# Optimization experiments

Hardware: AMD Instinct MI355X
Metric: run time of the kernel (lower is better)

The kernel has to match this reference:

```python
import jax, jax.numpy as jnp
import numpy as np

B, L, S, D, H, E, UV = 4, 2048, 2048, 1024, 8, 128, 128
ROT_DIM = H * E  # RotaryEmbedding(dim=qk_size*n_heads) applied on flattened dim


def gelu(x):
    return jax.nn.gelu(x, approximate=False)  # torch nn.GELU default (erf)


def rope(x):
    # x: [B, T, ROT_DIM]; interleaved-pair rotary (lucidrains rotary_embedding_torch default)
    T = x.shape[1]
    inv_freq = 1.0 / (10000.0 ** (jnp.arange(0, ROT_DIM, 2, dtype=jnp.float32) / ROT_DIM))
    freqs = jnp.arange(T, dtype=jnp.float32)[:, None] * inv_freq  # [T, ROT_DIM/2]
    cos = jnp.repeat(jnp.cos(freqs), 2, axis=-1)  # [T, ROT_DIM]
    sin = jnp.repeat(jnp.sin(freqs), 2, axis=-1)
    xp = x.reshape(*x.shape[:-1], ROT_DIM // 2, 2)
    x_rot = jnp.stack([-xp[..., 1], xp[..., 0]], axis=-1).reshape(x.shape)
    return x * cos + x_rot * sin


def setup_inputs() -> dict:
    key = jax.random.key(0)
    ks = jax.random.split(key, 16)
    n = lambda k, sh, s=1.0: jax.random.normal(k, sh, jnp.float32) * s
    w = 0.02
    return {
        "u": n(ks[0], (B, L, D)),
        "queries": n(ks[1], (B, L, D)),
        "keys": n(ks[2], (B, S, D)),
        "values": n(ks[3], (B, S, D)),
        "Wqk": n(ks[4], (D, H * E), w), "bqk": jnp.zeros((H * E,), jnp.float32),
        "Wv": n(ks[5], (D, H * UV), w), "bv": jnp.zeros((H * UV,), jnp.float32),
        "Wu": n(ks[6], (D, H * UV), w), "bu": jnp.zeros((H * UV,), jnp.float32),
        "Wo": n(ks[7], (H * UV, D), w), "bo": jnp.zeros((D,), jnp.float32),
        "q_gamma": jnp.ones((E,), jnp.float32), "q_beta": n(ks[8], (E,), w),
        "k_gamma": jnp.ones((E,), jnp.float32), "k_beta": n(ks[9], (E,), w),
    }


def _forward(u, queries, keys, values, Wqk, bqk, Wv, bv, Wu, bu, Wo, bo,
             q_gamma, q_beta, k_gamma, k_beta):
    # use_aff=True: shared qk projection + per-branch ScaleOffset over qk_size
    qk = gelu(queries @ Wqk + bqk)                      # [B,L,H*E]
    qk4 = qk.reshape(B, L, H, E)
    q = (qk4 * q_gamma + q_beta).reshape(B, L, H * E)
    k = (qk4 * k_gamma + k_beta).reshape(B, L, H * E)
    q = rope(q).reshape(B, L, H, E)
    k = rope(k).reshape(B, S, H, E)
    v = gelu(values @ Wv + bv).reshape(B, S, H, UV)
    # Conv1d(kernel_size=1) == pointwise linear over channels
    u_p = gelu(u @ Wu + bu).reshape(B, L, H, UV)
    scale = 1.0 / jnp.sqrt(jnp.float32(E))
    scores = jnp.einsum("blhe,bshe->bhls", q, k) * scale
    attn = jax.nn.softmax(scores, axis=-1)              # [B,H,L,S]
    ctx = jnp.einsum("bhls,bshd->blhd", attn, v)        # [B,L,H,UV]
    out = (u_p * ctx).reshape(B, L, H * UV)             # gate by u
    o = out @ Wo + bo                                   # [B,L,D]
    return o, attn


def reference(u, queries, keys, values, Wqk, bqk, Wv, bv, Wu, bu, Wo, bo,
              q_gamma, q_beta, k_gamma, k_beta):
    return _forward(u, queries, keys, values, Wqk, bqk, Wv, bv, Wu, bu, Wo, bo,
                    q_gamma, q_beta, k_gamma, k_beta)
```

## Files before the change

### kernel.cpp

```cpp
#include <hip/hip_runtime.h>
#include <hip/hip_bf16.h>
#include <math.h>

#define DEVI static __device__ __forceinline__

typedef __attribute__((ext_vector_type(4))) float f32x4;
typedef __attribute__((ext_vector_type(16))) float f32x16;
typedef __attribute__((ext_vector_type(8))) short bf16x8;
typedef __attribute__((ext_vector_type(4))) short bf16x4;

constexpr int Bc = 4, Lc = 2048, Sc = 2048, Dc = 1024, Hc = 8, Ec = 128, UVc = 128;
constexpr int HEc = Hc * Ec;
constexpr int BLc = Bc * Lc;

#define QSC (1.44269504088896340f / 11.31370849898476039f)

DEVI unsigned f2bf_bits(float f) {
  unsigned u = __builtin_bit_cast(unsigned, f);
  return (u + 0x7FFFu + ((u >> 16) & 1u)) >> 16;
}
DEVI short f2bf(float f) { return (short)f2bf_bits(f); }
DEVI float bf2f(short s) {
  return __builtin_bit_cast(float, (unsigned)((unsigned short)s) << 16);
}
DEVI float gelu_f(float x) {
  float z = fabsf(x) * 0.7071067811865476f;
  float t = __builtin_amdgcn_rcpf(1.0f + 0.3275911f * z);
  float p = t * (0.254829592f +
            t * (-0.284496736f +
            t * (1.421413741f +
            t * (-1.453152027f + t * 1.061405429f))));
  float e = exp2f(-z * z * 1.4426950408889634f);
  float er = copysignf(1.0f - p * e, x);
  return 0.5f * x * (1.0f + er);
}

DEVI void gload16(const void* gsrc, void* ldst) {
  __builtin_amdgcn_global_load_lds(
      (const __attribute__((address_space(1))) unsigned*)gsrc,
      (__attribute__((address_space(3))) unsigned*)(ldst), 16, 0, 0);
}

DEVI f32x4 mfma16(bf16x8 a, bf16x8 b, f32x4 c) {
  return __builtin_amdgcn_mfma_f32_16x16x32_bf16(a, b, c, 0, 0, 0);
}
DEVI f32x16 mfma32(bf16x8 a, bf16x8 b, f32x16 c) {
  return __builtin_amdgcn_mfma_f32_32x32x16_bf16(a, b, c, 0, 0, 0);
}

__global__ void prep_all_kernel(const float* __restrict__ in_q, const float* __restrict__ in_v,
                                const float* __restrict__ in_u, short* __restrict__ C1,
                                short* __restrict__ C2, short* __restrict__ C3,
                                const float* __restrict__ W0, const float* __restrict__ W1,
                                const float* __restrict__ W2, const float* __restrict__ W3,
                                short* __restrict__ T0, short* __restrict__ T1,
                                short* __restrict__ T2, short* __restrict__ T3,
                                float2* __restrict__ cs) {
  __shared__ float tbuf[32][33];
  const int bid = blockIdx.x;
  const int t = threadIdx.x;
  if (bid < 12288) {
    int which = bid >> 12, blk = bid & 4095;
    const float* in = (which == 0) ? in_q : (which == 1) ? in_v : in_u;
    short* out = (which == 0) ? C1 : (which == 1) ? C2 : C3;
    size_t i = ((size_t)blk * 256 + t) * 8;
    float4 f1 = *reinterpret_cast<const float4*>(in + i);
    float4 f2 = *reinterpret_cast<const float4*>(in + i + 4);
    uint4 pk;
    pk.x = f2bf_bits(f1.x) | (f2bf_bits(f1.y) << 16);
    pk.y = f2bf_bits(f1.z) | (f2bf_bits(f1.w) << 16);
    pk.z = f2bf_bits(f2.x) | (f2bf_bits(f2.y) << 16);
    pk.w = f2bf_bits(f2.z) | (f2bf_bits(f2.w) << 16);
    *reinterpret_cast<uint4*>(out + i) = pk;
  } else if (bid < 17408) {
    int z = (bid - 12288) >> 10, rem = (bid - 12288) & 1023;
    int n0 = (rem & 31) * 32, k0 = (rem >> 5) * 32;
    int tx = t & 31, ty = t >> 5;
    const float* Ws[4] = {W0, W1, W2, W3};
    short* Ts[4] = {T0, T1, T2, T3};
    const float* W = Ws[z];
    short* WT = Ts[z];
#pragma unroll
    for (int i = 0; i < 4; i++) {
      int r = ty + i * 8;
      tbuf[r][tx] = W[(size_t)(k0 + r) * 1024 + n0 + tx];
    }
    __syncthreads();
#pragma unroll
    for (int i = 0; i < 4; i++) {
      int r = ty + i * 8;
      WT[(size_t)(n0 + r) * 1024 + k0 + tx] = f2bf(tbuf[tx][r]);
    }
  } else {
    int base = (bid - 17408) * 256 + t;
#pragma unroll
    for (int j = 0; j < 4; j++) {
      int idx = base + j * 262144;
      int tt = idx >> 9, i = idx & 511;
      float inv = expf((float)i * (-9.210340371976184f / 512.0f));
      float sv, cv;
      sincosf((float)tt * inv, &sv, &cv);
      cs[idx] = make_float2(cv, sv);
    }
  }
}

template <int EPI>
DEVI void gemm_body(char* smem, int bx,
                    const short* __restrict__ A, const short* __restrict__ BT,
                    const float* __restrict__ bias, void* __restrict__ Cptr, int K, int N,
                    const float2* __restrict__ cstab,
                    const float* __restrict__ qg, const float* __restrict__ qb,
                    const float* __restrict__ kg, const float* __restrict__ kb,
                    short* __restrict__ qout, short* __restrict__ kout) {
  const int tid = threadIdx.x;
  const int wave = tid >> 6, lane = tid & 63;
  const int lquad = lane >> 4, l15 = lane & 15;
  const int m0 = (bx & 63) * 128, n0 = (bx >> 6) * 128;
  const int wr = wave >> 1, wc = wave & 1;
  f32x4 acc[4][4] = {};

  const int q0 = tid * 16, q1 = tid * 16 + 4096;
  const int r0 = q0 >> 6, o0 = (q0 & 63) ^ ((r0 & 3) << 4);
  const int r1 = q1 >> 6, o1 = (q1 & 63) ^ ((r1 & 3) << 4);
  const short* a0 = A + (size_t)(m0 + r0) * K + (o0 >> 1);
  const short* a1 = A + (size_t)(m0 + r1) * K + (o1 >> 1);
  const short* b0 = BT + (size_t)(n0 + r0) * K + (o0 >> 1);
  const short* b1 = BT + (size_t)(n0 + r1) * K + (o1 >> 1);

#define G_STAGE(buf, kt)                     \
  {                                          \
    char* As_ = smem + (buf)*8192;           \
    char* Bs_ = smem + 24576 + (buf)*8192;   \
    gload16(a0 + (kt), As_ + q0);            \
    gload16(a1 + (kt), As_ + q1);            \
    gload16(b0 + (kt), Bs_ + q0);            \
    gload16(b1 + (kt), Bs_ + q1);            \
  }

  G_STAGE(0, 0);
  G_STAGE(1, 32);
  asm volatile("s_waitcnt vmcnt(4)" ::: "memory");
  __builtin_amdgcn_s_barrier();

  const int NT = K >> 5;
  int cur = 0;
  for (int t = 0; t < NT; t++) {
    int nb = cur + 2;
    if (nb >= 3) nb -= 3;
    G_STAGE(nb, (t + 2 < NT) ? (t + 2) * 32 : 0);
    __builtin_amdgcn_sched_barrier(0);
    const char* As_ = smem + cur * 8192;
    const char* Bs_ = smem + 24576 + cur * 8192;
    const int ko = lquad * 16;
    bf16x8 a[4], b[4];
#pragma unroll
    for (int f = 0; f < 4; f++) {
      int ra = wr * 64 + f * 16 + l15;
      a[f] = *reinterpret_cast<const bf16x8*>(As_ + ra * 64 + (ko ^ ((ra & 3) << 4)));
      int rb = wc * 64 + f * 16 + l15;
      b[f] = *reinterpret_cast<const bf16x8*>(Bs_ + rb * 64 + (ko ^ ((rb & 3) << 4)));
    }
#pragma unroll
    for (int mf = 0; mf < 4; mf++)
#pragma unroll
      for (int nf = 0; nf < 4; nf++)
        acc[mf][nf] = mfma16(a[mf], b[nf], acc[mf][nf]);
    asm volatile("s_waitcnt vmcnt(4) lgkmcnt(0)" ::: "memory");
    __builtin_amdgcn_sched_barrier(0);
    __builtin_amdgcn_s_barrier();
    cur = (cur == 2) ? 0 : cur + 1;
  }
#undef G_STAGE

#pragma unroll
  for (int mf = 0; mf < 4; mf++) {
#pragma unroll
    for (int nf = 0; nf < 4; nf++) {
      const int mrow = m0 + wr * 64 + mf * 16 + 4 * lquad;
      const int ncol = n0 + wc * 64 + nf * 16 + l15;
      const float bval = bias[ncol];
      if constexpr (EPI == 2) {
        const int e7 = ncol & 127;
        const float QG = qg[e7], QB = qb[e7], KG = kg[e7], KB = kb[e7];
        const int p = ncol >> 1;
        const float sgn = (ncol & 1) ? 1.0f : -1.0f;
#pragma unroll
        for (int r = 0; r < 4; r++) {
          const int m = mrow + r;
          const int tt = m & 2047;
          float2 cs = cstab[(size_t)tt * 512 + p];
          float g = gelu_f(acc[mf][nf][r] + bval);
          float qv = g * QG + QB, kv = g * KG + KB;
          float pq = __shfl_xor(qv, 1), pk = __shfl_xor(kv, 1);
          qout[(size_t)m * HEc + ncol] = f2bf((qv * cs.x + sgn * pq * cs.y) * QSC);
          kout[(size_t)m * HEc + ncol] = f2bf(kv * cs.x + sgn * pk * cs.y);
        }
      } else if constexpr (EPI == 3) {
        int hh = ncol >> 7, dd = ncol & 127;
        int bb = mrow >> 11, ss = mrow & 2047;
        bf16x4 gv;
#pragma unroll
        for (int r = 0; r < 4; r++) gv[r] = f2bf(gelu_f(acc[mf][nf][r] + bval));
        *reinterpret_cast<bf16x4*>((short*)Cptr + (((size_t)bb * 8 + hh) * 128 + dd) * 2048 + ss) = gv;
      } else if constexpr (EPI == 1) {
#pragma unroll
        for (int r = 0; r < 4; r++)
          ((short*)Cptr)[(size_t)(mrow + r) * N + ncol] = f2bf(gelu_f(acc[mf][nf][r] + bval));
      } else {
#pragma unroll
        for (int r = 0; r < 4; r++)
          ((float*)Cptr)[(size_t)(mrow + r) * N + ncol] = acc[mf][nf][r] + bval;
      }
    }
  }
}

DEVI void passa_body(char* smem, int bid, const short* __restrict__ qs,
                     const short* __restrict__ ks, float* __restrict__ rcpbuf) {
  const int xcd = bid & 7, jj = bid >> 3;
  const int bh = xcd * 4 + (jj >> 4);
  const int lblk = jj & 15;
  const int b = bh >> 3, h = bh & 7;
  const int l0 = lblk * 128;
  const int tid = threadIdx.x;
  const int wave = tid >> 6, lane = tid & 63;
  const int l31 = lane & 31, lhg = lane >> 5;

  const short* ksrc[4];
  int kq[4];
#pragma unroll
  for (int i = 0; i < 4; i++) {
    int q = i * 4096 + tid * 16;
    kq[i] = q;
    int row = q >> 8, off = (q & 255) ^ ((row & 7) << 4);
    ksrc[i] = ks + (((size_t)b * Sc + row) * Hc + h) * Ec + (off >> 1);
  }

  bf16x8 qf[8];
  {
    const char* qp = (const char*)(qs + (((size_t)b * Lc + l0 + wave * 32 + l31) * Hc + h) * Ec);
#pragma unroll
    for (int kt = 0; kt < 8; kt++)
      qf[kt] = *reinterpret_cast<const bf16x8*>(qp + kt * 32 + 16 * lhg);
  }
  __builtin_amdgcn_sched_barrier(0);

#define STAGE_A(buf, s0)                                  \
  {                                                       \
    char* Kb_ = smem + (buf)*16384;                       \
    gload16(ksrc[0] + (size_t)(s0)*1024, Kb_ + kq[0]);    \
    gload16(ksrc[1] + (size_t)(s0)*1024, Kb_ + kq[1]);    \
    gload16(ksrc[2] + (size_t)(s0)*1024, Kb_ + kq[2]);    \
    gload16(ksrc[3] + (size_t)(s0)*1024, Kb_ + kq[3]);    \
  }

  STAGE_A(0, 0);
  STAGE_A(1, 64);
  asm volatile("s_waitcnt vmcnt(4)" ::: "memory");
  __builtin_amdgcn_s_barrier();
  float ra = 0.f, rb = 0.f, rc = 0.f, rd = 0.f;
  int cur = 0;
  for (int t = 0; t < 32; t++) {
    int nb = cur + 2;
    if (nb >= 3) nb -= 3;
    STAGE_A(nb, (t + 2 < 32) ? (t + 2) * 64 : 0);
    __builtin_amdgcn_sched_barrier(0);
    const char* KB_ = smem + cur * 16384;
    f32x16 d0 = {}, d1 = {};
    __builtin_amdgcn_s_setprio(1);
#pragma unroll
    for (int kt = 0; kt < 8; kt++) {
      int row0 = l31, row1 = 32 + l31;
      bf16x8 k0 = *reinterpret_cast<const bf16x8*>(
          KB_ + row0 * 256 + ((kt * 32 + 16 * lhg) ^ ((row0 & 7) << 4)));
      bf16x8 k1 = *reinterpret_cast<const bf16x8*>(
          KB_ + row1 * 256 + ((kt * 32 + 16 * lhg) ^ ((row1 & 7) << 4)));
      d0 = mfma32(k0, qf[kt], d0);
      d1 = mfma32(k1, qf[kt], d1);
    }
    __builtin_amdgcn_s_setprio(0);
#pragma unroll
    for (int r = 0; r < 16; r += 4) {
      ra += exp2f(d0[r]) + exp2f(d1[r]);
      rb += exp2f(d0[r + 1]) + exp2f(d1[r + 1]);
      rc += exp2f(d0[r + 2]) + exp2f(d1[r + 2]);
      rd += exp2f(d0[r + 3]) + exp2f(d1[r + 3]);
    }
    asm volatile("s_waitcnt vmcnt(4) lgkmcnt(0)" ::: "memory");
    __builtin_amdgcn_sched_barrier(0);
    __builtin_amdgcn_s_barrier();
    cur = (cur == 2) ? 0 : cur + 1;
  }
#undef STAGE_A
  float rs = (ra + rb) + (rc + rd);
  rs += __shfl_xor(rs, 32);
  if (lane < 32)
    rcpbuf[(size_t)bh * Lc + l0 + wave * 32 + l31] = 1.0f / rs;
}

__global__ __launch_bounds__(256, 3) void mid_kernel(
    const short* __restrict__ qs, const short* __restrict__ ks, float* __restrict__ rcpbuf,
    const short* __restrict__ C2, const short* __restrict__ WT1,
    const float* __restrict__ bv, short* __restrict__ vTb,
    const short* __restrict__ C3, const short* __restrict__ WT2,
    const float* __restrict__ bu, short* __restrict__ upb) {
  __shared__ char smem[49152];
  const int bid = blockIdx.x;
  if (bid < 512) {
    passa_body(smem, bid, qs, ks, rcpbuf);
  } else if (bid < 1024) {
    gemm_body<3>(smem, bid - 512, C2, WT1, bv, vTb, Dc, HEc,
                 nullptr, nullptr, nullptr, nullptr, nullptr, nullptr, nullptr);
  } else {
    gemm_body<1>(smem, bid - 1024, C3, WT2, bu, upb, Dc, HEc,
                 nullptr, nullptr, nullptr, nullptr, nullptr, nullptr, nullptr);
  }
}

__global__ __launch_bounds__(256, 3) void gemm_rope_kernel(
    const short* __restrict__ A, const short* __restrict__ BT,
    const float* __restrict__ bias, const float2* __restrict__ cstab,
    const float* __restrict__ qg, const float* __restrict__ qb,
    const float* __restrict__ kg, const float* __restrict__ kb,
    short* __restrict__ qout, short* __restrict__ kout) {
  __shared__ char smem[49152];
  gemm_body<2>(smem, blockIdx.x, A, BT, bias, nullptr, Dc, HEc,
               cstab, qg, qb, kg, kb, qout, kout);
}

__global__ __launch_bounds__(256, 3) void gemm_out_kernel(
    const short* __restrict__ A, const short* __restrict__ BT,
    const float* __restrict__ bias, float* __restrict__ C) {
  __shared__ char smem[49152];
  gemm_body<0>(smem, blockIdx.x, A, BT, bias, C, HEc, Dc,
               nullptr, nullptr, nullptr, nullptr, nullptr, nullptr, nullptr);
}

__global__ __launch_bounds__(256, 3) void attn_kernel(
    const short* __restrict__ qs, const short* __restrict__ ks,
    const short* __restrict__ vT, const short* __restrict__ up,
    const float* __restrict__ rcpbuf, float* __restrict__ attn_out,
    short* __restrict__ gate) {
  __shared__ char smem[49152];
  const int bid = blockIdx.x;
  const int xcd = bid & 7, jj = bid >> 3;
  const int bh = xcd * 4 + (jj >> 4);
  const int lblk = jj & 15;
  const int b = bh >> 3, h = bh & 7;
  const int l0 = lblk * 128;
  const int tid = threadIdx.x;
  const int wave = tid >> 6, lane = tid & 63;
  const int lquad = lane >> 4, l15 = lane & 15;

  const short* ksrc[2];
  int kq[2];
#pragma unroll
  for (int i = 0; i < 2; i++) {
    int q = i * 4096 + tid * 16;
    kq[i] = q;
    int row = q >> 8, off = (q & 255) ^ ((row & 7) << 4);
    ksrc[i] = ks + (((size_t)b * Sc + row) * Hc + h) * Ec + (off >> 1);
  }
  const short* vsrc[2];
  int vq[2];
#pragma unroll
  for (int i = 0; i < 2; i++) {
    int q = i * 4096 + tid * 16;
    vq[i] = q;
    int rv = q >> 6;
    int j = (q >> 4) & 3;
    int c = (j - (rv & 3)) & 3;
    vsrc[i] = vT + ((size_t)bh * UVc + rv) * Sc + (c << 3);
  }

  bf16x8 qf[2][4];
  float rcp[2];
#pragma unroll
  for (int cf = 0; cf < 2; cf++) {
    int lrow = l0 + wave * 32 + cf * 16 + l15;
    const short* qp = qs + (((size_t)b * Lc + lrow) * Hc + h) * Ec;
#pragma unroll
    for (int kt = 0; kt < 4; kt++)
      qf[cf][kt] = *reinterpret_cast<const bf16x8*>(qp + kt * 32 + lquad * 8);
    rcp[cf] = rcpbuf[(size_t)bh * Lc + lrow];
  }
  __builtin_amdgcn_sched_barrier(0);

#define STAGE_B(buf, s0)                                  \
  {                                                       \
    char* Kb_ = smem + (buf)*8192;                        \
    char* Vb_ = smem + 24576 + (buf)*8192;                \
    gload16(ksrc[0] + (size_t)(s0)*1024, Kb_ + kq[0]);    \
    gload16(ksrc[1] + (size_t)(s0)*1024, Kb_ + kq[1]);    \
    gload16(vsrc[0] + (s0), Vb_ + vq[0]);                 \
    gload16(vsrc[1] + (s0), Vb_ + vq[1]);                 \
  }

  STAGE_B(0, 0);
  STAGE_B(1, 32);
  asm volatile("s_waitcnt vmcnt(4)" ::: "memory");
  __builtin_amdgcn_s_barrier();
  f32x4 ctx[8][2] = {};
  int cur = 0;
  for (int t = 0; t < 64; t++) {
    const int s0 = t * 32;
    const char* KB_ = smem + cur * 8192;
    const char* VB_ = smem + 24576 + cur * 8192;
    f32x4 d[2][2] = {};
    __builtin_amdgcn_s_setprio(1);
#pragma unroll
    for (int kt = 0; kt < 4; kt++)
#pragma unroll
      for (int sf = 0; sf < 2; sf++) {
        int row = sf * 16 + l15;
        bf16x8 kf = *reinterpret_cast<const bf16x8*>(
            KB_ + row * 256 + ((kt * 64 + lquad * 16) ^ ((row & 7) << 4)));
        d[sf][0] = mfma16(kf, qf[0][kt], d[sf][0]);
        d[sf][1] = mfma16(kf, qf[1][kt], d[sf][1]);
      }
    __builtin_amdgcn_s_setprio(0);
#pragma unroll
    for (int sf = 0; sf < 2; sf++)
#pragma unroll
      for (int cf = 0; cf < 2; cf++)
#pragma unroll
        for (int r = 0; r < 4; r++)
          d[sf][cf][r] = exp2f(d[sf][cf][r]) * rcp[cf];
#pragma unroll
    for (int cf = 0; cf < 2; cf++) {
      int lrow = l0 + wave * 32 + cf * 16 + l15;
      float* arow = attn_out + ((size_t)bh * Lc + lrow) * Sc + s0 + lquad * 4;
      __builtin_nontemporal_store(d[0][cf], reinterpret_cast<f32x4*>(arow));
      __builtin_nontemporal_store(d[1][cf], reinterpret_cast<f32x4*>(arow + 16));
    }
    bf16x8 pb[2];
#pragma unroll
    for (int cf = 0; cf < 2; cf++)
#pragma unroll
      for (int r = 0; r < 4; r++) {
        pb[cf][r] = f2bf(d[0][cf][r]);
        pb[cf][4 + r] = f2bf(d[1][cf][r]);
      }
    __builtin_amdgcn_s_setprio(1);
#pragma unroll
    for (int df = 0; df < 8; df++) {
      int dd = df * 16 + l15;
      const char* vrow = VB_ + dd * 64;
      int half = (lquad & 1) * 8;
      int clo = ((lquad >> 1) + (dd & 3)) & 3;
      int chi = ((lquad >> 1) + 2 + (dd & 3)) & 3;
      bf16x4 lo = *reinterpret_cast<const bf16x4*>(vrow + clo * 16 + half);
      bf16x4 hi = *reinterpret_cast<const bf16x4*>(vrow + chi * 16 + half);
      bf16x8 vf = __builtin_shufflevector(lo, hi, 0, 1, 2, 3, 4, 5, 6, 7);
      ctx[df][0] = mfma16(vf, pb[0], ctx[df][0]);
      ctx[df][1] = mfma16(vf, pb[1], ctx[df][1]);
    }
    __builtin_amdgcn_s_setprio(0);
    {
      int nb = cur + 2;
      if (nb >= 3) nb -= 3;
      STAGE_B(nb, (t + 2 < 64) ? s0 + 64 : 0);
    }
    asm volatile("s_waitcnt vmcnt(8) lgkmcnt(0)" ::: "memory");
    __builtin_amdgcn_sched_barrier(0);
    __builtin_amdgcn_s_barrier();
    cur = (cur == 2) ? 0 : cur + 1;
  }
#undef STAGE_B

#pragma unroll
  for (int cf = 0; cf < 2; cf++) {
    int lrow = l0 + wave * 32 + cf * 16 + l15;
    size_t base = ((size_t)b * Lc + lrow) * HEc + h * UVc;
    const short* ub = up + base;
    short* gp = gate + base;
#pragma unroll
    for (int df = 0; df < 8; df++) {
      int doff = df * 16 + lquad * 4;
      bf16x4 uv = *reinterpret_cast<const bf16x4*>(ub + doff);
      bf16x4 gv;
#pragma unroll
      for (int r = 0; r < 4; r++)
        gv[r] = f2bf(bf2f(uv[r]) * ctx[df][cf][r]);
      *reinterpret_cast<bf16x4*>(gp + doff) = gv;
    }
  }
}

extern "C" void kernel_launch(void* const* d_in, const int* in_sizes, int n_in,
                              void* d_out, int out_size, void* d_ws, size_t ws_size,
                              hipStream_t stream) {
  const float* u_in = (const float*)d_in[0];
  const float* qry = (const float*)d_in[1];
  const float* vals = (const float*)d_in[3];
  const float* Wqk = (const float*)d_in[4];
  const float* bqk = (const float*)d_in[5];
  const float* Wv = (const float*)d_in[6];
  const float* bv = (const float*)d_in[7];
  const float* Wu = (const float*)d_in[8];
  const float* bu = (const float*)d_in[9];
  const float* Wo = (const float*)d_in[10];
  const float* bo = (const float*)d_in[11];
  const float* qg = (const float*)d_in[12];
  const float* qb = (const float*)d_in[13];
  const float* kg = (const float*)d_in[14];
  const float* kb = (const float*)d_in[15];

  char* w = (char*)d_ws;
  short* WT0 = (short*)w; w += (size_t)1024 * 1024 * 2;
  short* WT1 = (short*)w; w += (size_t)1024 * 1024 * 2;
  short* WT2 = (short*)w; w += (size_t)1024 * 1024 * 2;
  short* WT3 = (short*)w; w += (size_t)1024 * 1024 * 2;
  float2* cstab = (float2*)w; w += (size_t)2048 * 512 * 8;
  float* rcpb = (float*)w; w += (size_t)32 * 2048 * 4;
  const size_t BUF = (size_t)BLc * HEc * 2;
  short* C1 = (short*)w; w += BUF;
  short* C2 = (short*)w; w += BUF;
  short* C3 = (short*)w; w += BUF;
  short* qbf = (short*)w; w += BUF;
  short* kbf = (short*)w; w += BUF;
  short* vTb = (short*)w; w += BUF;
  short* upb = (short*)w; w += BUF;
  short* gtb = C1;

  float* o_out = (float*)d_out;
  float* attn_out = o_out + (size_t)BLc * Dc;

  prep_all_kernel<<<18432, 256, 0, stream>>>(qry, vals, u_in, C1, C2, C3, Wqk, Wv, Wu, Wo,
                                             WT0, WT1, WT2, WT3, cstab);
  gemm_rope_kernel<<<512, 256, 0, stream>>>(C1, WT0, bqk, cstab, qg, qb, kg, kb, qbf, kbf);
  mid_kernel<<<1536, 256, 0, stream>>>(qbf, kbf, rcpb, C2, WT1, bv, vTb, C3, WT2, bu, upb);
  attn_kernel<<<512, 256, 0, stream>>>(qbf, kbf, vTb, upb, rcpb, attn_out, gtb);
  gemm_out_kernel<<<512, 256, 0, stream>>>(gtb, WT3, bo, o_out);
}
```

Measured before the change: 365.0 us.

## Split prep kernel and overlap remaining conversions with QK rope GEMM

The monolithic prep kernel is split in two. The first kernel does only what the QK projection needs: converting queries, transposing Wqk and building the cos/sin table. The remaining conversions (values, u, Wv, Wu, Wo) run as extra blocks inside the rope GEMM launch, so this memory-bound work can overlap with the compute-bound GEMM instead of running before it. The risk is that the GEMM blocks now share the launch with many small blocks, and these compete for bandwidth and CU slots; the wt blocks also inherit the GEMM's large shared-memory allocation and launch bounds.

```diff
diff --git a/kernel.cpp b/kernel.cpp
--- a/kernel.cpp
+++ b/kernel.cpp
@@ -48,60 +48,45 @@
   return __builtin_amdgcn_mfma_f32_32x32x16_bf16(a, b, c, 0, 0, 0);
 }
 
-__global__ void prep_all_kernel(const float* __restrict__ in_q, const float* __restrict__ in_v,
-                                const float* __restrict__ in_u, short* __restrict__ C1,
-                                short* __restrict__ C2, short* __restrict__ C3,
-                                const float* __restrict__ W0, const float* __restrict__ W1,
-                                const float* __restrict__ W2, const float* __restrict__ W3,
-                                short* __restrict__ T0, short* __restrict__ T1,
-                                short* __restrict__ T2, short* __restrict__ T3,
-                                float2* __restrict__ cs) {
-  __shared__ float tbuf[32][33];
-  const int bid = blockIdx.x;
-  const int t = threadIdx.x;
-  if (bid < 12288) {
-    int which = bid >> 12, blk = bid & 4095;
-    const float* in = (which == 0) ? in_q : (which == 1) ? in_v : in_u;
-    short* out = (which == 0) ? C1 : (which == 1) ? C2 : C3;
-    size_t i = ((size_t)blk * 256 + t) * 8;
-    float4 f1 = *reinterpret_cast<const float4*>(in + i);
-    float4 f2 = *reinterpret_cast<const float4*>(in + i + 4);
-    uint4 pk;
-    pk.x = f2bf_bits(f1.x) | (f2bf_bits(f1.y) << 16);
-    pk.y = f2bf_bits(f1.z) | (f2bf_bits(f1.w) << 16);
-    pk.z = f2bf_bits(f2.x) | (f2bf_bits(f2.y) << 16);
-    pk.w = f2bf_bits(f2.z) | (f2bf_bits(f2.w) << 16);
-    *reinterpret_cast<uint4*>(out + i) = pk;
-  } else if (bid < 17408) {
-    int z = (bid - 12288) >> 10, rem = (bid - 12288) & 1023;
-    int n0 = (rem & 31) * 32, k0 = (rem >> 5) * 32;
-    int tx = t & 31, ty = t >> 5;
-    const float* Ws[4] = {W0, W1, W2, W3};
-    short* Ts[4] = {T0, T1, T2, T3};
-    const float* W = Ws[z];
-    short* WT = Ts[z];
-#pragma unroll
-    for (int i = 0; i < 4; i++) {
-      int r = ty + i * 8;
-      tbuf[r][tx] = W[(size_t)(k0 + r) * 1024 + n0 + tx];
-    }
-    __syncthreads();
-#pragma unroll
-    for (int i = 0; i < 4; i++) {
-      int r = ty + i * 8;
-      WT[(size_t)(n0 + r) * 1024 + k0 + tx] = f2bf(tbuf[tx][r]);
-    }
-  } else {
-    int base = (bid - 17408) * 256 + t;
-#pragma unroll
-    for (int j = 0; j < 4; j++) {
-      int idx = base + j * 262144;
-      int tt = idx >> 9, i = idx & 511;
-      float inv = expf((float)i * (-9.210340371976184f / 512.0f));
-      float sv, cv;
-      sincosf((float)tt * inv, &sv, &cv);
-      cs[idx] = make_float2(cv, sv);
-    }
+DEVI void cvt_body(int blk, int t, const float* __restrict__ in, short* __restrict__ out) {
+  size_t i = ((size_t)blk * 256 + t) * 8;
+  float4 f1 = *reinterpret_cast<const float4*>(in + i);
+  float4 f2 = *reinterpret_cast<const float4*>(in + i + 4);
+  uint4 pk;
+  pk.x = f2bf_bits(f1.x) | (f2bf_bits(f1.y) << 16);
+  pk.y = f2bf_bits(f1.z) | (f2bf_bits(f1.w) << 16);
+  pk.z = f2bf_bits(f2.x) | (f2bf_bits(f2.y) << 16);
+  pk.w = f2bf_bits(f2.z) | (f2bf_bits(f2.w) << 16);
+  *reinterpret_cast<uint4*>(out + i) = pk;
+}
+
+DEVI void wt_body(float (*tbuf)[33], int rem, int t, const float* __restrict__ W,
+                  short* __restrict__ WT) {
+  int n0 = (rem & 31) * 32, k0 = (rem >> 5) * 32;
+  int tx = t & 31, ty = t >> 5;
+#pragma unroll
+  for (int i = 0; i < 4; i++) {
+    int r = ty + i * 8;
+    tbuf[r][tx] = W[(size_t)(k0 + r) * 1024 + n0 + tx];
+  }
+  __syncthreads();
+#pragma unroll
+  for (int i = 0; i < 4; i++) {
+    int r = ty + i * 8;
+    WT[(size_t)(n0 + r) * 1024 + k0 + tx] = f2bf(tbuf[tx][r]);
+  }
+}
+
+DEVI void cstab_body(int blk, int t, float2* __restrict__ cs) {
+  int base = blk * 256 + t;
+#pragma unroll
+  for (int j = 0; j < 4; j++) {
+    int idx = base + j * 262144;
+    int tt = idx >> 9, i = idx & 511;
+    float inv = expf((float)i * (-9.210340371976184f / 512.0f));
+    float sv, cv;
+    sincosf((float)tt * inv, &sv, &cv);
+    cs[idx] = make_float2(cv, sv);
   }
 }
 
@@ -297,6 +282,49 @@
   rs += __shfl_xor(rs, 32);
   if (lane < 32)
     rcpbuf[(size_t)bh * Lc + l0 + wave * 32 + l31] = 1.0f / rs;
+}
+
+__global__ void prep1_kernel(const float* __restrict__ qry, short* __restrict__ C1,
+                             const float* __restrict__ Wqk, short* __restrict__ WT0,
+                             float2* __restrict__ cs) {
+  __shared__ float tbuf[32][33];
+  const int bid = blockIdx.x, t = threadIdx.x;
+  if (bid < 4096) {
+    cvt_body(bid, t, qry, C1);
+  } else if (bid < 5120) {
+    wt_body(tbuf, bid - 4096, t, Wqk, WT0);
+  } else {
+    cstab_body(bid - 5120, t, cs);
+  }
+}
+
+__global__ __launch_bounds__(256, 3) void rope_prep2_kernel(
+    const short* __restrict__ C1, const short* __restrict__ WT0,
+    const float* __restrict__ bqk, const float2* __restrict__ cstab,
+    const float* __restrict__ qg, const float* __restrict__ qb,
+    const float* __restrict__ kg, const float* __restrict__ kb,
+    short* __restrict__ qbf, short* __restrict__ kbf,
+    const float* __restrict__ vals, short* __restrict__ C2,
+    const float* __restrict__ u_in, short* __restrict__ C3,
+    const float* __restrict__ Wv, short* __restrict__ WT1,
+    const float* __restrict__ Wu, short* __restrict__ WT2,
+    const float* __restrict__ Wo, short* __restrict__ WT3) {
+  __shared__ char smem[49152];
+  const int bid = blockIdx.x, t = threadIdx.x;
+  if (bid < 512) {
+    gemm_body<2>(smem, bid, C1, WT0, bqk, nullptr, Dc, HEc,
+                 cstab, qg, qb, kg, kb, qbf, kbf);
+  } else if (bid < 4608) {
+    cvt_body(bid - 512, t, vals, C2);
+  } else if (bid < 8704) {
+    cvt_body(bid - 4608, t, u_in, C3);
+  } else if (bid < 9728) {
+    wt_body((float(*)[33])smem, bid - 8704, t, Wv, WT1);
+  } else if (bid < 10752) {
+    wt_body((float(*)[33])smem, bid - 9728, t, Wu, WT2);
+  } else {
+    wt_body((float(*)[33])smem, bid - 10752, t, Wo, WT3);
+  }
 }
 
 __global__ __launch_bounds__(256, 3) void mid_kernel(
@@ -316,17 +344,6 @@
     gemm_body<1>(smem, bid - 1024, C3, WT2, bu, upb, Dc, HEc,
                  nullptr, nullptr, nullptr, nullptr, nullptr, nullptr, nullptr);
   }
-}
-
-__global__ __launch_bounds__(256, 3) void gemm_rope_kernel(
-    const short* __restrict__ A, const short* __restrict__ BT,
-    const float* __restrict__ bias, const float2* __restrict__ cstab,
-    const float* __restrict__ qg, const float* __restrict__ qb,
-    const float* __restrict__ kg, const float* __restrict__ kb,
-    short* __restrict__ qout, short* __restrict__ kout) {
-  __shared__ char smem[49152];
-  gemm_body<2>(smem, blockIdx.x, A, BT, bias, nullptr, Dc, HEc,
-               cstab, qg, qb, kg, kb, qout, kout);
 }
 
 __global__ __launch_bounds__(256, 3) void gemm_out_kernel(
@@ -527,9 +544,10 @@
   float* o_out = (float*)d_out;
   float* attn_out = o_out + (size_t)BLc * Dc;
 
-  prep_all_kernel<<<18432, 256, 0, stream>>>(qry, vals, u_in, C1, C2, C3, Wqk, Wv, Wu, Wo,
-                                             WT0, WT1, WT2, WT3, cstab);
-  gemm_rope_kernel<<<512, 256, 0, stream>>>(C1, WT0, bqk, cstab, qg, qb, kg, kb, qbf, kbf);
+  prep1_kernel<<<6144, 256, 0, stream>>>(qry, C1, Wqk, WT0, cstab);
+  rope_prep2_kernel<<<11776, 256, 0, stream>>>(C1, WT0, bqk, cstab, qg, qb, kg, kb,
+                                               qbf, kbf, vals, C2, u_in, C3,
+                                               Wv, WT1, Wu, WT2, Wo, WT3);
   mid_kernel<<<1536, 256, 0, stream>>>(qbf, kbf, rcpb, C2, WT1, bv, vTb, C3, WT2, bu, upb);
   attn_kernel<<<512, 256, 0, stream>>>(qbf, kbf, vTb, upb, rcpb, attn_out, gtb);
   gemm_out_kernel<<<512, 256, 0, stream>>>(gtb, WT3, bo, o_out);
```

Result: no change. 362.0 us, median of 2 (-0.8%).
